# Kernel optimization log

Measured on AMD Instinct MI355X. Metric: run time of the kernel, lower is better.

The kernel has to match this reference:

```python
import jax, jax.numpy as jnp
import numpy as np

B, T, D_MODEL, D_HIDDEN, NUM_HEADS, K = 2, 4096, 1024, 2048, 4, 4
HEAD_DIM = D_HIDDEN // NUM_HEADS
LN_EPS = 1e-5


def setup_inputs() -> dict:
    key = jax.random.key(0)
    ks = jax.random.split(key, 12)
    x = jax.random.normal(ks[0], (B, T, D_MODEL), dtype=jnp.float32)
    def lin(k, din, dout, std=0.02):
        return jax.random.normal(k, (din, dout), dtype=jnp.float32) * std
    W_ih_w = lin(ks[1], D_MODEL, D_HIDDEN)
    W_ih_b = jnp.zeros((D_HIDDEN,), jnp.float32)
    W_gate_w = lin(ks[2], D_MODEL, D_HIDDEN)
    W_gate_b = jnp.zeros((D_HIDDEN,), jnp.float32)
    # selective decay: small weights, multi-scale per-head bias
    W_decay_w = lin(ks[3], D_MODEL, D_HIDDEN, std=0.01)
    scales = jnp.linspace(1.0, 5.5, NUM_HEADS)  # fast -> very slow decay
    W_decay_b = jnp.repeat(scales, HEAD_DIM).astype(jnp.float32)
    W_z_w = lin(ks[4], D_MODEL, D_HIDDEN)
    W_z_b = jnp.zeros((D_HIDDEN,), jnp.float32)
    conv_w = jax.random.normal(ks[5], (D_HIDDEN, K), dtype=jnp.float32) * (1.0 / np.sqrt(K))
    conv_b = jnp.zeros((D_HIDDEN,), jnp.float32)
    ln_g = jnp.ones((D_HIDDEN,), jnp.float32)
    ln_b = jnp.zeros((D_HIDDEN,), jnp.float32)
    W_out_w = lin(ks[6], D_HIDDEN, D_HIDDEN)
    W_out_b = jnp.zeros((D_HIDDEN,), jnp.float32)
    out_w = lin(ks[7], D_HIDDEN, D_MODEL)
    out_b = jnp.zeros((D_MODEL,), jnp.float32)
    return dict(x=x, W_ih_w=W_ih_w, W_ih_b=W_ih_b, W_gate_w=W_gate_w, W_gate_b=W_gate_b,
                W_decay_w=W_decay_w, W_decay_b=W_decay_b, W_z_w=W_z_w, W_z_b=W_z_b,
                conv_w=conv_w, conv_b=conv_b, ln_g=ln_g, ln_b=ln_b,
                W_out_w=W_out_w, W_out_b=W_out_b, out_w=out_w, out_b=out_b)


def _causal_depthwise_conv(u, conv_w, conv_b):
    # u: [B,T,C]; conv_w: [C,K]. Torch Conv1d(padding=K-1)[..., :T] == left-pad causal conv.
    t = u.shape[1]
    k = conv_w.shape[1]
    up = jnp.pad(u, ((0, 0), (k - 1, 0), (0, 0)))
    out = conv_b
    for j in range(k):  # small fixed K, unrolled
        out = out + conv_w[:, j] * up[:, j:j + t, :]
    return out


def _linear_scan(alpha, beta):
    # inclusive scan of h_t = alpha_t * h_{t-1} + beta_t, h_{-1}=0, along axis 1
    def comb(c1, c2):
        a1, b1 = c1
        a2, b2 = c2
        return (a1 * a2, b1 * a2 + b2)
    _, h = jax.lax.associative_scan(comb, (alpha, beta), axis=1)
    return h


def reference(x, W_ih_w, W_ih_b, W_gate_w, W_gate_b, W_decay_w, W_decay_b,
              W_z_w, W_z_b, conv_w, conv_b, ln_g, ln_b, W_out_w, W_out_b, out_w, out_b):
    ih = x @ W_ih_w + W_ih_b                       # [B,T,H]
    ih = _causal_depthwise_conv(ih, conv_w, conv_b)
    gate = jax.nn.sigmoid(x @ W_gate_w + W_gate_b)
    a = jax.nn.sigmoid(x @ W_decay_w + W_decay_b)
    z = jax.nn.silu(x @ W_z_w + W_z_b)
    alpha = (1.0 - gate) * a
    beta = gate * ih
    h = _linear_scan(alpha, beta)                  # selective linear recurrence
    mu = jnp.mean(h, axis=-1, keepdims=True)
    var = jnp.mean(jnp.square(h - mu), axis=-1, keepdims=True)
    hn = (h - mu) * jax.lax.rsqrt(var + LN_EPS) * ln_g + ln_b
    out = z * hn
    out = out @ W_out_w + W_out_b
    return out @ out_w + out_b
```

## Files before the change

kernel.cpp:

```cpp
#include <hip/hip_runtime.h>
#include <hip/hip_bf16.h>

#define B_  2
#define T_  4096
#define DM  1024
#define DH  2048
#define M_  (B_*T_)
#define NC  64
#define CL  64

typedef __bf16 bf16x8 __attribute__((ext_vector_type(8)));
typedef float  f32x4  __attribute__((ext_vector_type(4)));
typedef unsigned short ushort_t;
typedef unsigned int   uint_t;

__device__ __forceinline__ float sigmoidf_(float v) { return 1.f / (1.f + __expf(-v)); }

__device__ __forceinline__ ushort_t f2bf_rne(float x) {
    uint_t u = __float_as_uint(x);
    uint_t r = (u + 0x7fffu + ((u >> 16) & 1u)) >> 16;
    return (ushort_t)r;
}
__device__ __forceinline__ float bf2f(ushort_t h) {
    return __uint_as_float(((uint_t)h) << 16);
}
__device__ __forceinline__ void hl_split(float x, ushort_t& h, ushort_t& l) {
    h = f2bf_rne(x);
    l = f2bf_rne(x - bf2f(h));
}

__device__ __forceinline__ void gload16(const ushort_t* g, ushort_t* l) {
    __builtin_amdgcn_global_load_lds((const __attribute__((address_space(1))) void*)g,
                                     (__attribute__((address_space(3))) void*)l,
                                     16, 0, 0);
}

__global__ __launch_bounds__(256)
void split_hi_lo(const float* __restrict__ src, ushort_t* __restrict__ hi,
                 ushort_t* __restrict__ lo)
{
    int gid = blockIdx.x * 256 + threadIdx.x;
    float4 v = ((const float4*)src)[gid];
    ushort4 h, l;
    hl_split(v.x, h.x, l.x);
    hl_split(v.y, h.y, l.y);
    hl_split(v.z, h.z, l.z);
    hl_split(v.w, h.w, l.w);
    ((ushort4*)hi)[gid] = h;
    ((ushort4*)lo)[gid] = l;
}

__global__ __launch_bounds__(256)
void split_t(const float* __restrict__ src, ushort_t* __restrict__ dhi,
             ushort_t* __restrict__ dlo, int R, int C)
{
    __shared__ float tile[32][33];
    int tid = threadIdx.x;
    int c0 = blockIdx.x * 32, r0 = blockIdx.y * 32;
    int tr = tid >> 3, tc = (tid & 7) * 4;
    float4 v = *(const float4*)(src + (size_t)(r0 + tr) * C + c0 + tc);
    tile[tc + 0][tr] = v.x;
    tile[tc + 1][tr] = v.y;
    tile[tc + 2][tr] = v.z;
    tile[tc + 3][tr] = v.w;
    __syncthreads();
    int orr = tid >> 3, oc = (tid & 7) * 4;
    ushort4 h, l;
    hl_split(tile[orr][oc + 0], h.x, l.x);
    hl_split(tile[orr][oc + 1], h.y, l.y);
    hl_split(tile[orr][oc + 2], h.z, l.z);
    hl_split(tile[orr][oc + 3], h.w, l.w);
    *(ushort4*)(dhi + (size_t)(c0 + orr) * R + r0 + oc) = h;
    *(ushort4*)(dlo + (size_t)(c0 + orr) * R + r0 + oc) = l;
}

template<int ACT>
__global__ __launch_bounds__(256)
void mfma_gemm(const ushort_t* __restrict__ Ahg, const ushort_t* __restrict__ Alg,
               const ushort_t* __restrict__ Bhg, const ushort_t* __restrict__ Blg,
               int K,
               float* __restrict__ C0, const float* __restrict__ bias,
               const float* __restrict__ aux,
               ushort_t* __restrict__ Uhi, ushort_t* __restrict__ Ulo)
{
    __shared__ __align__(16) ushort_t Ah[128][32];
    __shared__ __align__(16) ushort_t Al[128][32];
    __shared__ __align__(16) ushort_t Bh[128][32];
    __shared__ __align__(16) ushort_t Bl[128][32];

    const int tid = threadIdx.x;
    int nwg = gridDim.x * gridDim.y;
    int bid = blockIdx.y * gridDim.x + blockIdx.x;
    int swz = (bid & 7) * (nwg >> 3) + (bid >> 3);
    int bx = swz % gridDim.x, by = swz / gridDim.x;
    const int n0 = bx * 128, m0 = by * 128;

    const int r_ = tid >> 2;
    const int s_ = tid & 3;
    const int wv = tid >> 6, wr = wv >> 1, wc = wv & 1;
    const int lr = tid & 15, lg = (tid >> 4) & 3;
    const int sl = lg ^ ((lr >> 1) & 3);

    f32x4 acc[4][4];
#pragma unroll
    for (int i = 0; i < 4; i++)
#pragma unroll
        for (int j = 0; j < 4; j++) acc[i][j] = (f32x4){0.f, 0.f, 0.f, 0.f};

    for (int kt = 0; kt < K; kt += 32) {
#pragma unroll
        for (int c = 0; c < 2; c++) {
            const int row   = r_ + (c << 6);
            const int sslot = s_ ^ ((row >> 1) & 3);
            const size_t ga = (size_t)(m0 + row) * K + kt + (sslot << 3);
            const size_t gb = (size_t)(n0 + row) * K + kt + (sslot << 3);
            const int lrow  = (wv << 4) + (c << 6);
            gload16(Ahg + ga, &Ah[lrow][0]);
            gload16(Alg + ga, &Al[lrow][0]);
            gload16(Bhg + gb, &Bh[lrow][0]);
            gload16(Blg + gb, &Bl[lrow][0]);
        }
        __syncthreads();
        bf16x8 a_h[4], a_l[4], b_h[4], b_l[4];
#pragma unroll
        for (int i = 0; i < 4; i++) {
            a_h[i] = *(const bf16x8*)&Ah[wr * 64 + i * 16 + lr][sl * 8];
            a_l[i] = *(const bf16x8*)&Al[wr * 64 + i * 16 + lr][sl * 8];
            b_h[i] = *(const bf16x8*)&Bh[wc * 64 + i * 16 + lr][sl * 8];
            b_l[i] = *(const bf16x8*)&Bl[wc * 64 + i * 16 + lr][sl * 8];
        }
#pragma unroll
        for (int i = 0; i < 4; i++)
#pragma unroll
            for (int j = 0; j < 4; j++) {
                acc[i][j] = __builtin_amdgcn_mfma_f32_16x16x32_bf16(a_h[i], b_h[j], acc[i][j], 0, 0, 0);
                acc[i][j] = __builtin_amdgcn_mfma_f32_16x16x32_bf16(a_h[i], b_l[j], acc[i][j], 0, 0, 0);
                acc[i][j] = __builtin_amdgcn_mfma_f32_16x16x32_bf16(a_l[i], b_h[j], acc[i][j], 0, 0, 0);
            }
        __syncthreads();
    }

    const int N = gridDim.x * 128;
#pragma unroll
    for (int i = 0; i < 4; i++)
#pragma unroll
        for (int j = 0; j < 4; j++) {
            int n = n0 + wc * 64 + j * 16 + lr;
            float bv = bias ? bias[n] : 0.f;
#pragma unroll
            for (int rr = 0; rr < 4; rr++) {
                int m = m0 + wr * 64 + i * 16 + lg * 4 + rr;
                float v = acc[i][j][rr] + bv;
                if (ACT == 1) {
                    v = sigmoidf_(v);
                } else if (ACT == 2) {
                    v = sigmoidf_(v) * (1.f - aux[(size_t)m * N + n]);
                } else if (ACT == 3) {
                    float zz = v * sigmoidf_(v);
                    float uu = zz * aux[(size_t)m * N + n];
                    ushort_t uh, ul;
                    hl_split(uu, uh, ul);
                    Uhi[(size_t)m * N + n] = uh;
                    Ulo[(size_t)m * N + n] = ul;
                }
                if (ACT != 3) C0[(size_t)m * N + n] = v;
            }
        }
}

__global__ __launch_bounds__(256)
void conv_beta(const float* __restrict__ ihp, float* gate_beta,
               const float* __restrict__ cw, const float* __restrict__ cb)
{
    int gid = blockIdx.x * 256 + threadIdx.x;
    int c4  = gid & 511;
    int row = gid >> 9;
    int t   = row & (T_ - 1);
    const float4* ih4 = (const float4*)ihp;
    float4 g = ((const float4*)gate_beta)[gid];
    int c0 = c4 * 4;
    float4 w0 = ((const float4*)cw)[c0 + 0];
    float4 w1 = ((const float4*)cw)[c0 + 1];
    float4 w2 = ((const float4*)cw)[c0 + 2];
    float4 w3 = ((const float4*)cw)[c0 + 3];
    float4 cbv = ((const float4*)cb)[c4];
    float4 v[4];
#pragma unroll
    for (int j = 0; j < 4; j++) {
        int tt = t + j - 3;
        if (tt >= 0) v[j] = ih4[(size_t)(row + j - 3) * 512 + c4];
        else         v[j] = make_float4(0.f, 0.f, 0.f, 0.f);
    }
    float4 ihc;
    ihc.x = cbv.x + w0.x * v[0].x + w0.y * v[1].x + w0.z * v[2].x + w0.w * v[3].x;
    ihc.y = cbv.y + w1.x * v[0].y + w1.y * v[1].y + w1.z * v[2].y + w1.w * v[3].y;
    ihc.z = cbv.z + w2.x * v[0].z + w2.y * v[1].z + w2.z * v[2].z + w2.w * v[3].z;
    ihc.w = cbv.w + w3.x * v[0].w + w3.y * v[1].w + w3.z * v[2].w + w3.w * v[3].w;
    float4 beta;
    beta.x = g.x * ihc.x;  beta.y = g.y * ihc.y;
    beta.z = g.z * ihc.z;  beta.w = g.w * ihc.w;
    ((float4*)gate_beta)[gid] = beta;
}

__global__ __launch_bounds__(256)
void scan_phaseA(const float* __restrict__ alpha, const float* __restrict__ beta,
                 float* __restrict__ sA, float* __restrict__ sB)
{
    int gid  = blockIdx.x * 256 + threadIdx.x;
    int c    = gid & (DH - 1);
    int rest = gid >> 11;
    int chunk = rest & (NC - 1);
    int b    = rest >> 6;
    size_t base = ((size_t)(b * T_ + chunk * CL)) * DH + c;
    float Ar = 1.f, Br = 0.f;
    for (int l = 0; l < CL; l++) {
        float al = alpha[base + (size_t)l * DH];
        float be = beta [base + (size_t)l * DH];
        Ar *= al;
        Br = Br * al + be;
    }
    int si = chunk * (B_ * DH) + b * DH + c;
    sA[si] = Ar; sB[si] = Br;
}

__global__ __launch_bounds__(256)
void scan_phaseB(const float* __restrict__ sA, const float* __restrict__ sB,
                 float* __restrict__ hinit)
{
    int gid = blockIdx.x * 256 + threadIdx.x;
    int c = gid & (DH - 1); int b = gid >> 11;
    float h = 0.f;
    for (int ch = 0; ch < NC; ch++) {
        int si = ch * (B_ * DH) + b * DH + c;
        hinit[si] = h;
        h = sA[si] * h + sB[si];
    }
}

__global__ __launch_bounds__(256)
void scan_phaseC(const float* __restrict__ alpha, const float* beta,
                 const float* __restrict__ hinit, float* hout)
{
    int gid  = blockIdx.x * 256 + threadIdx.x;
    int c    = gid & (DH - 1);
    int rest = gid >> 11;
    int chunk = rest & (NC - 1);
    int b    = rest >> 6;
    size_t base = ((size_t)(b * T_ + chunk * CL)) * DH + c;
    float h = hinit[chunk * (B_ * DH) + b * DH + c];
    for (int l = 0; l < CL; l++) {
        float al = alpha[base + (size_t)l * DH];
        float be = beta [base + (size_t)l * DH];
        h = al * h + be;
        hout[base + (size_t)l * DH] = h;
    }
}

__global__ __launch_bounds__(256)
void ln_inplace(float* h, const float* __restrict__ g, const float* __restrict__ bl)
{
    int row = blockIdx.x;
    int tid = threadIdx.x;
    float4* h4 = (float4*)(h + (size_t)row * DH);
    float4 v0 = h4[tid], v1 = h4[tid + 256];
    float s = v0.x + v0.y + v0.z + v0.w + v1.x + v1.y + v1.z + v1.w;
    float q = v0.x * v0.x + v0.y * v0.y + v0.z * v0.z + v0.w * v0.w
            + v1.x * v1.x + v1.y * v1.y + v1.z * v1.z + v1.w * v1.w;
#pragma unroll
    for (int o = 32; o; o >>= 1) { s += __shfl_down(s, o); q += __shfl_down(q, o); }
    __shared__ float rs[4], rq[4];
    int wid = tid >> 6, lane = tid & 63;
    if (lane == 0) { rs[wid] = s; rq[wid] = q; }
    __syncthreads();
    s = rs[0] + rs[1] + rs[2] + rs[3];
    q = rq[0] + rq[1] + rq[2] + rq[3];
    float mu  = s * (1.f / DH);
    float var = q * (1.f / DH) - mu * mu;
    float ri  = rsqrtf(var + 1e-5f);
    const float4* g4 = (const float4*)g;
    const float4* b4 = (const float4*)bl;
    {
        float4 gg = g4[tid], bb = b4[tid], o;
        o.x = (v0.x - mu) * ri * gg.x + bb.x;
        o.y = (v0.y - mu) * ri * gg.y + bb.y;
        o.z = (v0.z - mu) * ri * gg.z + bb.z;
        o.w = (v0.w - mu) * ri * gg.w + bb.w;
        h4[tid] = o;
    }
    {
        float4 gg = g4[tid + 256], bb = b4[tid + 256], o;
        o.x = (v1.x - mu) * ri * gg.x + bb.x;
        o.y = (v1.y - mu) * ri * gg.y + bb.y;
        o.z = (v1.z - mu) * ri * gg.z + bb.z;
        o.w = (v1.w - mu) * ri * gg.w + bb.w;
        h4[tid + 256] = o;
    }
}

__global__ __launch_bounds__(256)
void bc_kernel(const float* __restrict__ wob, const float* __restrict__ ow,
               const float* __restrict__ ob, float* __restrict__ bc)
{
    int n = blockIdx.x * 256 + threadIdx.x;
    float acc = ob[n];
    for (int k = 0; k < DH; k++) acc += wob[k] * ow[(size_t)k * DM + n];
    bc[n] = acc;
}

extern "C" void kernel_launch(void* const* d_in, const int* in_sizes, int n_in,
                              void* d_out, int out_size, void* d_ws, size_t ws_size,
                              hipStream_t stream)
{
    const float* x   = (const float*)d_in[0];
    const float* Wih = (const float*)d_in[1];
    const float* bih = (const float*)d_in[2];
    const float* Wg  = (const float*)d_in[3];
    const float* bg  = (const float*)d_in[4];
    const float* Wd  = (const float*)d_in[5];
    const float* bd  = (const float*)d_in[6];
    const float* Wz  = (const float*)d_in[7];
    const float* bz  = (const float*)d_in[8];
    const float* cw  = (const float*)d_in[9];
    const float* cb  = (const float*)d_in[10];
    const float* lng = (const float*)d_in[11];
    const float* lnb = (const float*)d_in[12];
    const float* Wow = (const float*)d_in[13];
    const float* Wob = (const float*)d_in[14];
    const float* ow  = (const float*)d_in[15];
    const float* ob  = (const float*)d_in[16];
    float* out = (float*)d_out;

    char* p = (char*)d_ws;
    float* R0 = (float*)(p);
    float* R1 = (float*)(p + ((size_t)64  << 20));
    float* R2 = (float*)(p + ((size_t)128 << 20));
    ushort_t* Wsh = (ushort_t*)(p + ((size_t)192 << 20));
    ushort_t* Wsl = (ushort_t*)(p + ((size_t)200 << 20));
    float* sA    = (float*)(p + ((size_t)208 << 20));
    float* sB    = (float*)(p + ((size_t)209 << 20));
    float* hinit = (float*)(p + ((size_t)210 << 20));
    float* bc    = (float*)(p + ((size_t)211 << 20));
    ushort_t* xhi = (ushort_t*)d_out;
    ushort_t* xlo = (ushort_t*)((char*)d_out + ((size_t)16 << 20));
    ushort_t* wowh = (ushort_t*)R0;
    ushort_t* wowl = (ushort_t*)((char*)R0 + ((size_t)8  << 20));
    ushort_t* owth = (ushort_t*)((char*)R0 + ((size_t)16 << 20));
    ushort_t* owtl = (ushort_t*)((char*)R0 + ((size_t)20 << 20));
    float*    Wc   = (float*)   ((char*)R0 + ((size_t)24 << 20));
    ushort_t* Wcth = (ushort_t*)((char*)R0 + ((size_t)32 << 20));
    ushort_t* Wctl = (ushort_t*)((char*)R0 + ((size_t)36 << 20));
    ushort_t* uhi = (ushort_t*)R2;
    ushort_t* ulo = (ushort_t*)((char*)R2 + ((size_t)32 << 20));

    split_hi_lo<<<(M_ * DM / 4) / 256, 256, 0, stream>>>(x, xhi, xlo);

    split_t<<<dim3(DH / 32, DM / 32), 256, 0, stream>>>(Wih, Wsh, Wsl, DM, DH);
    mfma_gemm<0><<<dim3(DH / 128, M_ / 128), 256, 0, stream>>>(
        xhi, xlo, Wsh, Wsl, DM, R0, bih, nullptr, nullptr, nullptr);

    split_t<<<dim3(DH / 32, DM / 32), 256, 0, stream>>>(Wg, Wsh, Wsl, DM, DH);
    mfma_gemm<1><<<dim3(DH / 128, M_ / 128), 256, 0, stream>>>(
        xhi, xlo, Wsh, Wsl, DM, R1, bg, nullptr, nullptr, nullptr);

    split_t<<<dim3(DH / 32, DM / 32), 256, 0, stream>>>(Wd, Wsh, Wsl, DM, DH);
    mfma_gemm<2><<<dim3(DH / 128, M_ / 128), 256, 0, stream>>>(
        xhi, xlo, Wsh, Wsl, DM, R2, bd, R1, nullptr, nullptr);

    conv_beta<<<(M_ * DH / 4) / 256, 256, 0, stream>>>(R0, R1, cw, cb);

    scan_phaseA<<<(B_ * DH * NC) / 256, 256, 0, stream>>>(R2, R1, sA, sB);
    scan_phaseB<<<(B_ * DH) / 256, 256, 0, stream>>>(sA, sB, hinit);
    scan_phaseC<<<(B_ * DH * NC) / 256, 256, 0, stream>>>(R2, R1, hinit, R1);

    ln_inplace<<<M_, 256, 0, stream>>>(R1, lng, lnb);

    split_hi_lo<<<((size_t)DH * DH / 4) / 256, 256, 0, stream>>>(Wow, wowh, wowl);
    split_t<<<dim3(DM / 32, DH / 32), 256, 0, stream>>>(ow, owth, owtl, DH, DM);
    mfma_gemm<0><<<dim3(DM / 128, DH / 128), 256, 0, stream>>>(
        wowh, wowl, owth, owtl, DH, Wc, nullptr, nullptr, nullptr, nullptr);
    split_t<<<dim3(DM / 32, DH / 32), 256, 0, stream>>>(Wc, Wcth, Wctl, DH, DM);
    bc_kernel<<<DM / 256, 256, 0, stream>>>(Wob, ow, ob, bc);

    split_t<<<dim3(DH / 32, DM / 32), 256, 0, stream>>>(Wz, Wsh, Wsl, DM, DH);
    mfma_gemm<3><<<dim3(DH / 128, M_ / 128), 256, 0, stream>>>(
        xhi, xlo, Wsh, Wsl, DM, nullptr, bz, R1, uhi, ulo);

    mfma_gemm<0><<<dim3(DM / 128, M_ / 128), 256, 0, stream>>>(
        uhi, ulo, Wcth, Wctl, DH, out, bc, nullptr, nullptr, nullptr);
}
```

Measured before the change: 998.4 us.

## Double-buffer LDS tiles in MFMA GEMM to overlap global loads with compute

Doubles the shared-memory tile buffers in the split-bf16 MFMA GEMM and issues the next K-tile's global-to-LDS loads before computing on the current tile. This removes one barrier per iteration and is meant to hide global load latency behind the MFMA work. LDS use per block doubles, which may reduce occupancy. Correctness depends on the async loads being complete before the barrier at the end of each iteration.

```diff
diff --git a/kernel.cpp b/kernel.cpp
--- a/kernel.cpp
+++ b/kernel.cpp
@@ -83,10 +83,10 @@
                const float* __restrict__ aux,
                ushort_t* __restrict__ Uhi, ushort_t* __restrict__ Ulo)
 {
-    __shared__ __align__(16) ushort_t Ah[128][32];
-    __shared__ __align__(16) ushort_t Al[128][32];
-    __shared__ __align__(16) ushort_t Bh[128][32];
-    __shared__ __align__(16) ushort_t Bl[128][32];
+    __shared__ __align__(16) ushort_t Ah[2][128][32];
+    __shared__ __align__(16) ushort_t Al[2][128][32];
+    __shared__ __align__(16) ushort_t Bh[2][128][32];
+    __shared__ __align__(16) ushort_t Bl[2][128][32];
 
     const int tid = threadIdx.x;
     int nwg = gridDim.x * gridDim.y;
@@ -97,37 +97,44 @@
 
     const int r_ = tid >> 2;
     const int s_ = tid & 3;
+    const int sslot = s_ ^ ((r_ >> 1) & 3);
     const int wv = tid >> 6, wr = wv >> 1, wc = wv & 1;
     const int lr = tid & 15, lg = (tid >> 4) & 3;
     const int sl = lg ^ ((lr >> 1) & 3);
 
+    auto STAGE = [&](int buf, int kt) {
+#pragma unroll
+        for (int c = 0; c < 2; c++) {
+            const size_t ga = (size_t)(m0 + r_ + (c << 6)) * K + kt + (sslot << 3);
+            const size_t gb = (size_t)(n0 + r_ + (c << 6)) * K + kt + (sslot << 3);
+            const int lrow  = (wv << 4) + (c << 6);
+            gload16(Ahg + ga, &Ah[buf][lrow][0]);
+            gload16(Alg + ga, &Al[buf][lrow][0]);
+            gload16(Bhg + gb, &Bh[buf][lrow][0]);
+            gload16(Blg + gb, &Bl[buf][lrow][0]);
+        }
+    };
+
     f32x4 acc[4][4];
 #pragma unroll
     for (int i = 0; i < 4; i++)
 #pragma unroll
         for (int j = 0; j < 4; j++) acc[i][j] = (f32x4){0.f, 0.f, 0.f, 0.f};
 
-    for (int kt = 0; kt < K; kt += 32) {
-#pragma unroll
-        for (int c = 0; c < 2; c++) {
-            const int row   = r_ + (c << 6);
-            const int sslot = s_ ^ ((row >> 1) & 3);
-            const size_t ga = (size_t)(m0 + row) * K + kt + (sslot << 3);
-            const size_t gb = (size_t)(n0 + row) * K + kt + (sslot << 3);
-            const int lrow  = (wv << 4) + (c << 6);
-            gload16(Ahg + ga, &Ah[lrow][0]);
-            gload16(Alg + ga, &Al[lrow][0]);
-            gload16(Bhg + gb, &Bh[lrow][0]);
-            gload16(Blg + gb, &Bl[lrow][0]);
-        }
-        __syncthreads();
+    const int nT = K >> 5;
+    STAGE(0, 0);
+    __syncthreads();
+
+    int cur = 0;
+    for (int t = 0; t < nT; ++t) {
+        if (t + 1 < nT) STAGE(cur ^ 1, (t + 1) << 5);
         bf16x8 a_h[4], a_l[4], b_h[4], b_l[4];
 #pragma unroll
         for (int i = 0; i < 4; i++) {
-            a_h[i] = *(const bf16x8*)&Ah[wr * 64 + i * 16 + lr][sl * 8];
-            a_l[i] = *(const bf16x8*)&Al[wr * 64 + i * 16 + lr][sl * 8];
-            b_h[i] = *(const bf16x8*)&Bh[wc * 64 + i * 16 + lr][sl * 8];
-            b_l[i] = *(const bf16x8*)&Bl[wc * 64 + i * 16 + lr][sl * 8];
+            a_h[i] = *(const bf16x8*)&Ah[cur][wr * 64 + i * 16 + lr][sl * 8];
+            a_l[i] = *(const bf16x8*)&Al[cur][wr * 64 + i * 16 + lr][sl * 8];
+            b_h[i] = *(const bf16x8*)&Bh[cur][wc * 64 + i * 16 + lr][sl * 8];
+            b_l[i] = *(const bf16x8*)&Bl[cur][wc * 64 + i * 16 + lr][sl * 8];
         }
 #pragma unroll
         for (int i = 0; i < 4; i++)
@@ -138,6 +145,7 @@
                 acc[i][j] = __builtin_amdgcn_mfma_f32_16x16x32_bf16(a_l[i], b_h[j], acc[i][j], 0, 0, 0);
             }
         __syncthreads();
+        cur ^= 1;
     }
 
     const int N = gridDim.x * 128;
```

Measured after the change: 929.4 us. 1.07x faster.
